# Performance work log

Measured on AMD Instinct MI355X. Metric: run time of the kernel, lower is better.

## Reference

```python
import jax, jax.numpy as jnp
import numpy as np

B, C, D, K = 65536, 128, 32, 10
EPS = 1e-12


def setup_inputs() -> dict:
    key = jax.random.key(0)
    k1, k2, k3, k4 = jax.random.split(key, 4)
    data = jax.random.normal(k1, (B, D), dtype=jnp.float32)
    mu = jax.random.normal(k2, (C, D), dtype=jnp.float32)
    # S_inv must be symmetric positive definite (inverse covariance per cluster)
    A = 0.1 * jax.random.normal(k3, (C, D, D), dtype=jnp.float32)
    S_inv = jnp.einsum('cij,ckj->cik', A, A) + jnp.eye(D, dtype=jnp.float32)[None]
    # one-hot class assignment per cluster (int32), as stored in the module
    cls = jax.random.randint(k4, (C,), 0, K)
    cluster_labels = jax.nn.one_hot(cls, K, dtype=jnp.int32)
    return {"data": data, "mu": mu, "S_inv": S_inv, "cluster_labels": cluster_labels}


def reference(data, mu, S_inv, cluster_labels):
    # Mahalanobis distance d2[b,c] = (z_b - mu_c)^T S_inv_c (z_b - mu_c),
    # expanded to avoid a [B, C, D] diff tensor.
    zz = data[:, :, None] * data[:, None, :]            # [B, D, D]
    t1 = jnp.einsum('bde,cde->bc', zz, S_inv)           # z' Sinv z
    Sm = jnp.einsum('cde,ce->cd', S_inv, mu)            # [C, D]
    t2 = data @ Sm.T                                    # z' Sinv mu  [B, C]
    t3 = jnp.einsum('cd,cd->c', mu, Sm)                 # mu' Sinv mu [C]
    d2 = t1 - 2.0 * t2 + t3[None, :]                    # [B, C]
    Gamma = jnp.exp(-0.5 * d2)                          # Gaussian activation
    # defuzzify_batch: normalize activations, project through one-hot labels
    norm_gamma = Gamma / (jnp.sum(Gamma, axis=1, keepdims=True) + EPS)
    label_scores = norm_gamma @ cluster_labels.astype(jnp.float32)  # [B, K]
    preds = jnp.argmax(label_scores, axis=1)
    clusters = jnp.argmax(Gamma, axis=1)
    return label_scores, preds, clusters
```

## Files before the change

### kernel.cpp

```cpp
#include <hip/hip_runtime.h>
#include <cmath>

#define B_N 65536
#define C_N 128
#define D_N 32
#define K_N 10
#define EPS_F 1e-12f
#define SCALE_F (-0.72134752044448169f)

#define NKK 48
#define CHUNK_F16 4096
#define QF_N (NKK * CHUNK_F16)
#define YSTR 33

typedef _Float16 f16x8 __attribute__((ext_vector_type(8)));
typedef float    f32x16 __attribute__((ext_vector_type(16)));

__device__ __forceinline__ void mdkk(int kk, int& dA, int& e0) {
    if (kk >= 45) { dA = 0; e0 = 0; return; }
    int w = (kk >= 17) + (kk >= 30) + (kk >= 39) + (kk >= 44);
    int off = w == 0 ? 0 : (w == 1 ? 17 : (w == 2 ? 30 : (w == 3 ? 39 : 44)));
    int r = kk - off;
    dA = 2 * r;
    e0 = 2 * r + 8 * w;
}

__global__ __launch_bounds__(128) void k_prep(const float* __restrict__ S,
                                              const float* __restrict__ mu,
                                              const int* __restrict__ onehot,
                                              _Float16* __restrict__ QF,
                                              int* __restrict__ cls) {
    const int c = blockIdx.x;
    const int tid = threadIdx.x;
    __shared__ float sSm[D_N];
    __shared__ float st3;

    if (tid < D_N) {
        const float* Sr = S + (size_t)c * (D_N * D_N) + (size_t)tid * D_N;
        const float* mr = mu + (size_t)c * D_N;
        float a0 = 0.f, a1 = 0.f;
#pragma unroll
        for (int e = 0; e < D_N; e += 2) {
            a0 = fmaf(Sr[e + 0], mr[e + 0], a0);
            a1 = fmaf(Sr[e + 1], mr[e + 1], a1);
        }
        sSm[tid] = a0 + a1;
    }
    __syncthreads();
    if (tid == 0) {
        const float* mr = mu + (size_t)c * D_N;
        float a = 0.f;
#pragma unroll
        for (int d = 0; d < D_N; ++d) a = fmaf(mr[d], sSm[d], a);
        st3 = a;
        int cl = 0;
#pragma unroll
        for (int k = 0; k < K_N; ++k)
            if (onehot[c * K_N + k] != 0) cl = k;
        cls[c] = cl;
    }
    __syncthreads();

    if (tid < 2 * NKK) {
        const int kk   = tid >> 1;
        const int half = tid & 1;
        int dA, e0;
        mdkk(kk, dA, e0);
        const int d  = dA + half;
        const int ct = c >> 5;
        const size_t base = (size_t)kk * CHUNK_F16 + ct * 1024
                          + (size_t)(half * 32 + (c & 31)) * 8;
        const float* Sc = S + (size_t)c * (D_N * D_N);
        for (int j = 0; j < 8; ++j) {
            const int e = e0 + j;
            float q = 0.f;
            if (kk < 45 && d <= e && e <= 32) {
                float v;
                if (e < 32)      v = Sc[d * D_N + e] * (d == e ? 1.f : 2.f);
                else if (d < 32) v = -2.f * sSm[d];
                else             v = st3;
                q = SCALE_F * v;
            }
            _Float16 h = (_Float16)q;
            QF[base + j]       = h;
            QF[base + 512 + j] = (_Float16)(q - (float)h);
        }
    }
}

__device__ __forceinline__ void gl_lds16(const void* g, void* l) {
    __builtin_amdgcn_global_load_lds(
        (const __attribute__((address_space(1))) unsigned int*)g,
        (__attribute__((address_space(3))) unsigned int*)l, 16, 0, 0);
}

__device__ __forceinline__ void stage_chunk(const _Float16* __restrict__ QF,
                                            _Float16* __restrict__ dst,
                                            int chunk, int wid, int lane) {
#pragma unroll
    for (int i = 0; i < 2; ++i) {
        const int slot = i * 4 + wid;
        gl_lds16(QF + (size_t)chunk * CHUNK_F16 + slot * 512 + lane * 8,
                 dst + slot * 512);
    }
}

__device__ __forceinline__ void ldy(const float* sy, int ybase, int hioff,
                                    int kk, float& yd, float (&yw)[8]) {
    int dA, e0;
    mdkk(kk, dA, e0);
    yd = sy[ybase + dA + hioff];
#pragma unroll
    for (int j = 0; j < 8; ++j) yw[j] = sy[ybase + e0 + j];
}

__device__ __forceinline__ void mkphi(float yd, const float (&yw)[8],
                                      f16x8& ph, f16x8& pl) {
    union { unsigned int w[4]; f16x8 v; } H, L;
#pragma unroll
    for (int p = 0; p < 4; ++p) {
        float f0 = yd * yw[2 * p], f1 = yd * yw[2 * p + 1];
        auto h2 = __builtin_amdgcn_cvt_pkrtz(f0, f1);
        float r0 = f0 - (float)h2[0];
        float r1 = f1 - (float)h2[1];
        auto l2 = __builtin_amdgcn_cvt_pkrtz(r0, r1);
        __builtin_memcpy(&H.w[p], &h2, 4);
        __builtin_memcpy(&L.w[p], &l2, 4);
    }
    ph = H.v;
    pl = L.v;
}

template <int SN, int SS, int P>
__device__ __forceinline__ void phase_t(int t, const _Float16* __restrict__ QF,
                                        _Float16* __restrict__ qb,
                                        const float* __restrict__ sy,
                                        int ybase, int hioff, int wid, int lane,
                                        f16x8 (&qh)[2][4], f16x8 (&ql)[2][4],
                                        float (&yd)[2], float (&yw)[2][8],
                                        f32x16 (&acc)[4]) {
    asm volatile("s_waitcnt vmcnt(0)" ::: "memory");
    __builtin_amdgcn_s_barrier();
    __builtin_amdgcn_sched_barrier(0);
    if (t + 2 < NKK)
        stage_chunk(QF, qb + SS * CHUNK_F16, t + 2, wid, lane);
    if (t + 1 < NKK) {
        const f16x8* qn = (const f16x8*)(qb + SN * CHUNK_F16);
#pragma unroll
        for (int ct = 0; ct < 4; ++ct) {
            qh[P ^ 1][ct] = qn[ct * 128 + lane];
            ql[P ^ 1][ct] = qn[ct * 128 + 64 + lane];
        }
        ldy(sy, ybase, hioff, t + 1, yd[P ^ 1], yw[P ^ 1]);
    }
    f16x8 ph, pl;
    mkphi(yd[P], yw[P], ph, pl);
    __builtin_amdgcn_s_setprio(1);
#pragma unroll
    for (int ct = 0; ct < 4; ++ct)
        acc[ct] = __builtin_amdgcn_mfma_f32_32x32x16_f16(qh[P][ct], ph, acc[ct], 0, 0, 0);
#pragma unroll
    for (int ct = 0; ct < 4; ++ct)
        acc[ct] = __builtin_amdgcn_mfma_f32_32x32x16_f16(ql[P][ct], ph, acc[ct], 0, 0, 0);
#pragma unroll
    for (int ct = 0; ct < 4; ++ct)
        acc[ct] = __builtin_amdgcn_mfma_f32_32x32x16_f16(qh[P][ct], pl, acc[ct], 0, 0, 0);
    __builtin_amdgcn_s_setprio(0);
}

__global__ __launch_bounds__(256, 2) void k_mainv9(const float* __restrict__ data,
                                                   const _Float16* __restrict__ QF,
                                                   const int* __restrict__ clsp,
                                                   float* __restrict__ out) {
    const int tid  = threadIdx.x;
    const int lane = tid & 63;
    const int wid  = tid >> 6;
    const int b0w  = blockIdx.x * 128 + wid * 32;
    const int col  = lane & 31;
    const bool hi  = lane >= 32;

    __shared__ float sy[256 * YSTR + 64];
    __shared__ alignas(16) _Float16 qb[4 * CHUNK_F16];
    __shared__ int lcls[C_N];
    if (tid < C_N) lcls[tid] = clsp[tid];

    const int ybase = tid * YSTR;
    {
        const float4* p0 = (const float4*)(data + (size_t)(b0w + col) * D_N);
#pragma unroll
        for (int i = 0; i < 8; ++i) {
            float4 v = p0[i];
            sy[ybase + 4 * i + 0] = v.x;
            sy[ybase + 4 * i + 1] = v.y;
            sy[ybase + 4 * i + 2] = v.z;
            sy[ybase + 4 * i + 3] = v.w;
        }
        sy[ybase + 32] = 1.f;
        if (tid < 64) sy[256 * YSTR + tid] = 0.f;
    }

    f32x16 acc[4];
#pragma unroll
    for (int ct = 0; ct < 4; ++ct)
#pragma unroll
        for (int g = 0; g < 16; ++g) acc[ct][g] = 0.f;

    stage_chunk(QF, qb + 0 * CHUNK_F16, 0, wid, lane);
    stage_chunk(QF, qb + 1 * CHUNK_F16, 1, wid, lane);
    __syncthreads();

    const int hioff = hi ? 1 : 0;
    f16x8 qh[2][4], ql[2][4];
    float yd[2], yw[2][8];
    {
        const f16x8* q0 = (const f16x8*)qb;
#pragma unroll
        for (int ct = 0; ct < 4; ++ct) {
            qh[0][ct] = q0[ct * 128 + lane];
            ql[0][ct] = q0[ct * 128 + 64 + lane];
        }
        ldy(sy, ybase, hioff, 0, yd[0], yw[0]);
    }

#pragma clang loop unroll(disable)
    for (int t = 0; t < NKK; t += 4) {
        phase_t<1, 2, 0>(t + 0, QF, qb, sy, ybase, hioff, wid, lane, qh, ql, yd, yw, acc);
        phase_t<2, 3, 1>(t + 1, QF, qb, sy, ybase, hioff, wid, lane, qh, ql, yd, yw, acc);
        phase_t<3, 0, 0>(t + 2, QF, qb, sy, ybase, hioff, wid, lane, qh, ql, yd, yw, acc);
        phase_t<0, 1, 1>(t + 3, QF, qb, sy, ybase, hioff, wid, lane, qh, ql, yd, yw, acc);
    }

    const float hoff = hi ? 4.f : 0.f;
    const int* lc = lcls + (hi ? 4 : 0);
    float sum = 0.f, gmax = -1.f, gcf = 0.f;
    float a0 = 0, a1 = 0, a2 = 0, a3 = 0, a4 = 0, a5 = 0, a6 = 0, a7 = 0, a8 = 0, a9 = 0;
#pragma unroll
    for (int ct = 0; ct < 4; ++ct) {
        float psum = 0.f;
#pragma unroll
        for (int g = 0; g < 16; ++g) {
            float v = acc[ct][g];
            float gm;
            asm("v_exp_f32 %0, %1" : "=v"(gm) : "v"(v));
            const int cbase = ct * 32 + (g & 3) + 8 * (g >> 2);
            int cl = lc[cbase];
            psum += gm;
            float cf = (float)cbase + hoff;
            if (gm > gmax) { gmax = gm; gcf = cf; }
            a0 += (cl == 0) ? gm : 0.f;
            a1 += (cl == 1) ? gm : 0.f;
            a2 += (cl == 2) ? gm : 0.f;
            a3 += (cl == 3) ? gm : 0.f;
            a4 += (cl == 4) ? gm : 0.f;
            a5 += (cl == 5) ? gm : 0.f;
            a6 += (cl == 6) ? gm : 0.f;
            a7 += (cl == 7) ? gm : 0.f;
            a8 += (cl == 8) ? gm : 0.f;
            a9 += (cl == 9) ? gm : 0.f;
        }
        sum += psum;
    }

    sum += __shfl_xor(sum, 32, 64);
    {
        float om = __shfl_xor(gmax, 32, 64);
        float oc = __shfl_xor(gcf, 32, 64);
        bool take = (om > gmax) || (om == gmax && oc < gcf);
        if (take) { gmax = om; gcf = oc; }
    }
    a0 += __shfl_xor(a0, 32, 64);
    a1 += __shfl_xor(a1, 32, 64);
    a2 += __shfl_xor(a2, 32, 64);
    a3 += __shfl_xor(a3, 32, 64);
    a4 += __shfl_xor(a4, 32, 64);
    a5 += __shfl_xor(a5, 32, 64);
    a6 += __shfl_xor(a6, 32, 64);
    a7 += __shfl_xor(a7, 32, 64);
    a8 += __shfl_xor(a8, 32, 64);
    a9 += __shfl_xor(a9, 32, 64);

    if (!hi) {
        const int b = b0w + col;
        float inv = 1.0f / (sum + EPS_F);
        float ls[K_N] = {a0 * inv, a1 * inv, a2 * inv, a3 * inv, a4 * inv,
                         a5 * inv, a6 * inv, a7 * inv, a8 * inv, a9 * inv};
        float best = -1.f;
        int bk = 0;
#pragma unroll
        for (int k = 0; k < K_N; ++k)
            if (ls[k] > best) { best = ls[k]; bk = k; }
        float2* o2 = (float2*)(out + (size_t)b * K_N);
#pragma unroll
        for (int k2 = 0; k2 < K_N / 2; ++k2)
            o2[k2] = make_float2(ls[2 * k2], ls[2 * k2 + 1]);
        out[(size_t)B_N * K_N + b] = (float)bk;
        out[(size_t)B_N * K_N + B_N + b] = gcf;
    }
}

extern "C" void kernel_launch(void* const* d_in, const int* in_sizes, int n_in,
                              void* d_out, int out_size, void* d_ws, size_t ws_size,
                              hipStream_t stream) {
    const float* data   = (const float*)d_in[0];
    const float* mu     = (const float*)d_in[1];
    const float* S      = (const float*)d_in[2];
    const int*   onehot = (const int*)d_in[3];
    float* out = (float*)d_out;

    _Float16* QF  = (_Float16*)d_ws;
    int*      cls = (int*)(QF + QF_N);

    hipLaunchKernelGGL(k_prep, dim3(C_N), dim3(128), 0, stream,
                       S, mu, onehot, QF, cls);
    hipLaunchKernelGGL(k_mainv9, dim3(B_N / 128), dim3(256), 0, stream,
                       data, QF, cls, out);
}
```

Before: 109.9 us.

## Split cluster columns across two waves per row group with 512-thread blocks

Blocks grow from 4 to 8 waves. Each pair of waves covers the same 32 rows but half of the 128 clusters, so each wave holds 2 accumulator tiles instead of 4 and more waves can be resident. The y operand loads become a sliding window that reuses the previous values instead of reloading 8 floats every step, and the software-pipelined register double buffering of Q fragments is removed. Partial sums, maxima and class sums from the two column halves are merged through a shared-memory scratch with an extra block barrier. Q staging now spreads one LDS load per wave across 8 waves.

```diff
diff --git a/kernel.cpp b/kernel.cpp
--- a/kernel.cpp
+++ b/kernel.cpp
@@ -94,26 +94,6 @@
         (__attribute__((address_space(3))) unsigned int*)l, 16, 0, 0);
 }
 
-__device__ __forceinline__ void stage_chunk(const _Float16* __restrict__ QF,
-                                            _Float16* __restrict__ dst,
-                                            int chunk, int wid, int lane) {
-#pragma unroll
-    for (int i = 0; i < 2; ++i) {
-        const int slot = i * 4 + wid;
-        gl_lds16(QF + (size_t)chunk * CHUNK_F16 + slot * 512 + lane * 8,
-                 dst + slot * 512);
-    }
-}
-
-__device__ __forceinline__ void ldy(const float* sy, int ybase, int hioff,
-                                    int kk, float& yd, float (&yw)[8]) {
-    int dA, e0;
-    mdkk(kk, dA, e0);
-    yd = sy[ybase + dA + hioff];
-#pragma unroll
-    for (int j = 0; j < 8; ++j) yw[j] = sy[ybase + e0 + j];
-}
-
 __device__ __forceinline__ void mkphi(float yd, const float (&yw)[8],
                                       f16x8& ph, f16x8& pl) {
     union { unsigned int w[4]; f16x8 v; } H, L;
@@ -131,103 +111,94 @@
     pl = L.v;
 }
 
-template <int SN, int SS, int P>
-__device__ __forceinline__ void phase_t(int t, const _Float16* __restrict__ QF,
-                                        _Float16* __restrict__ qb,
-                                        const float* __restrict__ sy,
-                                        int ybase, int hioff, int wid, int lane,
-                                        f16x8 (&qh)[2][4], f16x8 (&ql)[2][4],
-                                        float (&yd)[2], float (&yw)[2][8],
-                                        f32x16 (&acc)[4]) {
-    asm volatile("s_waitcnt vmcnt(0)" ::: "memory");
-    __builtin_amdgcn_s_barrier();
-    __builtin_amdgcn_sched_barrier(0);
-    if (t + 2 < NKK)
-        stage_chunk(QF, qb + SS * CHUNK_F16, t + 2, wid, lane);
-    if (t + 1 < NKK) {
-        const f16x8* qn = (const f16x8*)(qb + SN * CHUNK_F16);
-#pragma unroll
-        for (int ct = 0; ct < 4; ++ct) {
-            qh[P ^ 1][ct] = qn[ct * 128 + lane];
-            ql[P ^ 1][ct] = qn[ct * 128 + 64 + lane];
-        }
-        ldy(sy, ybase, hioff, t + 1, yd[P ^ 1], yw[P ^ 1]);
-    }
-    f16x8 ph, pl;
-    mkphi(yd[P], yw[P], ph, pl);
-    __builtin_amdgcn_s_setprio(1);
-#pragma unroll
-    for (int ct = 0; ct < 4; ++ct)
-        acc[ct] = __builtin_amdgcn_mfma_f32_32x32x16_f16(qh[P][ct], ph, acc[ct], 0, 0, 0);
-#pragma unroll
-    for (int ct = 0; ct < 4; ++ct)
-        acc[ct] = __builtin_amdgcn_mfma_f32_32x32x16_f16(ql[P][ct], ph, acc[ct], 0, 0, 0);
-#pragma unroll
-    for (int ct = 0; ct < 4; ++ct)
-        acc[ct] = __builtin_amdgcn_mfma_f32_32x32x16_f16(qh[P][ct], pl, acc[ct], 0, 0, 0);
-    __builtin_amdgcn_s_setprio(0);
-}
-
-__global__ __launch_bounds__(256, 2) void k_mainv9(const float* __restrict__ data,
-                                                   const _Float16* __restrict__ QF,
-                                                   const int* __restrict__ clsp,
-                                                   float* __restrict__ out) {
+__global__ __launch_bounds__(512, 4) void k_mainv10(const float* __restrict__ data,
+                                                    const _Float16* __restrict__ QF,
+                                                    const int* __restrict__ clsp,
+                                                    float* __restrict__ out) {
     const int tid  = threadIdx.x;
     const int lane = tid & 63;
     const int wid  = tid >> 6;
-    const int b0w  = blockIdx.x * 128 + wid * 32;
+    const int rg   = wid >> 1;
+    const int cg   = wid & 1;
     const int col  = lane & 31;
     const bool hi  = lane >= 32;
-
-    __shared__ float sy[256 * YSTR + 64];
+    const int bb   = blockIdx.x * 128;
+
+    __shared__ float sy[128 * YSTR + 64];
     __shared__ alignas(16) _Float16 qb[4 * CHUNK_F16];
     __shared__ int lcls[C_N];
+    __shared__ float scr[4][2][32][14];
+
     if (tid < C_N) lcls[tid] = clsp[tid];
-
-    const int ybase = tid * YSTR;
-    {
-        const float4* p0 = (const float4*)(data + (size_t)(b0w + col) * D_N);
+    if (tid < 128) {
+        const float4* p0 = (const float4*)(data + (size_t)(bb + tid) * D_N);
+        const int yb = tid * YSTR;
 #pragma unroll
         for (int i = 0; i < 8; ++i) {
             float4 v = p0[i];
-            sy[ybase + 4 * i + 0] = v.x;
-            sy[ybase + 4 * i + 1] = v.y;
-            sy[ybase + 4 * i + 2] = v.z;
-            sy[ybase + 4 * i + 3] = v.w;
-        }
-        sy[ybase + 32] = 1.f;
-        if (tid < 64) sy[256 * YSTR + tid] = 0.f;
-    }
-
-    f32x16 acc[4];
-#pragma unroll
-    for (int ct = 0; ct < 4; ++ct)
-#pragma unroll
-        for (int g = 0; g < 16; ++g) acc[ct][g] = 0.f;
-
-    stage_chunk(QF, qb + 0 * CHUNK_F16, 0, wid, lane);
-    stage_chunk(QF, qb + 1 * CHUNK_F16, 1, wid, lane);
+            sy[yb + 4 * i + 0] = v.x;
+            sy[yb + 4 * i + 1] = v.y;
+            sy[yb + 4 * i + 2] = v.z;
+            sy[yb + 4 * i + 3] = v.w;
+        }
+        sy[yb + 32] = 1.f;
+    } else if (tid < 192) {
+        sy[128 * YSTR + (tid - 128)] = 0.f;
+    }
+
+    f32x16 acc[2];
+#pragma unroll
+    for (int lt = 0; lt < 2; ++lt)
+#pragma unroll
+        for (int g = 0; g < 16; ++g) acc[lt][g] = 0.f;
+
+    gl_lds16(QF + 0 * CHUNK_F16 + wid * 512 + lane * 8, qb + 0 * CHUNK_F16 + wid * 512);
+    gl_lds16(QF + 1 * CHUNK_F16 + wid * 512 + lane * 8, qb + 1 * CHUNK_F16 + wid * 512);
     __syncthreads();
 
     const int hioff = hi ? 1 : 0;
-    f16x8 qh[2][4], ql[2][4];
-    float yd[2], yw[2][8];
-    {
-        const f16x8* q0 = (const f16x8*)qb;
-#pragma unroll
-        for (int ct = 0; ct < 4; ++ct) {
-            qh[0][ct] = q0[ct * 128 + lane];
-            ql[0][ct] = q0[ct * 128 + 64 + lane];
-        }
-        ldy(sy, ybase, hioff, 0, yd[0], yw[0]);
-    }
+    const float* yrow = sy + (rg * 32 + col) * YSTR;
+    float yw[8], yd = 0.f;
+    int e0 = 0, dAh = hioff;
 
 #pragma clang loop unroll(disable)
-    for (int t = 0; t < NKK; t += 4) {
-        phase_t<1, 2, 0>(t + 0, QF, qb, sy, ybase, hioff, wid, lane, qh, ql, yd, yw, acc);
-        phase_t<2, 3, 1>(t + 1, QF, qb, sy, ybase, hioff, wid, lane, qh, ql, yd, yw, acc);
-        phase_t<3, 0, 0>(t + 2, QF, qb, sy, ybase, hioff, wid, lane, qh, ql, yd, yw, acc);
-        phase_t<0, 1, 1>(t + 3, QF, qb, sy, ybase, hioff, wid, lane, qh, ql, yd, yw, acc);
+    for (int t = 0; t < NKK; ++t) {
+        asm volatile("s_waitcnt vmcnt(0)" ::: "memory");
+        __builtin_amdgcn_s_barrier();
+        __builtin_amdgcn_sched_barrier(0);
+        if (t + 2 < NKK)
+            gl_lds16(QF + (size_t)(t + 2) * CHUNK_F16 + wid * 512 + lane * 8,
+                     qb + ((t + 2) & 3) * CHUNK_F16 + wid * 512);
+
+        if (t == 0 || t == 17 || t == 30 || t == 39 || t == 44) {
+            e0  = (t == 0) ? 0 : (t == 17) ? 8 : (t == 30) ? 16 : (t == 39) ? 24 : 32;
+            dAh = hioff;
+#pragma unroll
+            for (int j = 0; j < 8; ++j) yw[j] = yrow[e0 + j];
+            yd = yrow[dAh];
+        } else if (t < 45) {
+            e0 += 2; dAh += 2;
+            yw[0] = yw[2]; yw[1] = yw[3]; yw[2] = yw[4];
+            yw[3] = yw[5]; yw[4] = yw[6]; yw[5] = yw[7];
+            yw[6] = yrow[e0 + 6];
+            yw[7] = yrow[e0 + 7];
+            yd = yrow[dAh];
+        }
+
+        const f16x8* qc = (const f16x8*)(qb + ((t & 3) * CHUNK_F16) + cg * 2048);
+        f16x8 qh0 = qc[lane],       ql0 = qc[64 + lane];
+        f16x8 qh1 = qc[128 + lane], ql1 = qc[192 + lane];
+
+        f16x8 ph, pl;
+        mkphi(yd, yw, ph, pl);
+        __builtin_amdgcn_s_setprio(1);
+        acc[0] = __builtin_amdgcn_mfma_f32_32x32x16_f16(qh0, ph, acc[0], 0, 0, 0);
+        acc[1] = __builtin_amdgcn_mfma_f32_32x32x16_f16(qh1, ph, acc[1], 0, 0, 0);
+        acc[0] = __builtin_amdgcn_mfma_f32_32x32x16_f16(ql0, ph, acc[0], 0, 0, 0);
+        acc[1] = __builtin_amdgcn_mfma_f32_32x32x16_f16(ql1, ph, acc[1], 0, 0, 0);
+        acc[0] = __builtin_amdgcn_mfma_f32_32x32x16_f16(qh0, pl, acc[0], 0, 0, 0);
+        acc[1] = __builtin_amdgcn_mfma_f32_32x32x16_f16(qh1, pl, acc[1], 0, 0, 0);
+        __builtin_amdgcn_s_setprio(0);
     }
 
     const float hoff = hi ? 4.f : 0.f;
@@ -235,14 +206,15 @@
     float sum = 0.f, gmax = -1.f, gcf = 0.f;
     float a0 = 0, a1 = 0, a2 = 0, a3 = 0, a4 = 0, a5 = 0, a6 = 0, a7 = 0, a8 = 0, a9 = 0;
 #pragma unroll
-    for (int ct = 0; ct < 4; ++ct) {
+    for (int lt = 0; lt < 2; ++lt) {
+        const int gt = cg * 2 + lt;
         float psum = 0.f;
 #pragma unroll
         for (int g = 0; g < 16; ++g) {
-            float v = acc[ct][g];
+            float v = acc[lt][g];
             float gm;
             asm("v_exp_f32 %0, %1" : "=v"(gm) : "v"(v));
-            const int cbase = ct * 32 + (g & 3) + 8 * (g >> 2);
+            const int cbase = gt * 32 + (g & 3) + 8 * (g >> 2);
             int cl = lc[cbase];
             psum += gm;
             float cf = (float)cbase + hoff;
@@ -280,21 +252,36 @@
     a9 += __shfl_xor(a9, 32, 64);
 
     if (!hi) {
-        const int b = b0w + col;
-        float inv = 1.0f / (sum + EPS_F);
-        float ls[K_N] = {a0 * inv, a1 * inv, a2 * inv, a3 * inv, a4 * inv,
-                         a5 * inv, a6 * inv, a7 * inv, a8 * inv, a9 * inv};
+        float* s = scr[rg][cg][col];
+        s[0] = sum; s[1] = gmax; s[2] = gcf;
+        s[3] = a0; s[4] = a1; s[5] = a2; s[6] = a3; s[7] = a4;
+        s[8] = a5; s[9] = a6; s[10] = a7; s[11] = a8; s[12] = a9;
+    }
+    __syncthreads();
+
+    if (cg == 0 && !hi) {
+        const float* s0 = scr[rg][0][col];
+        const float* s1 = scr[rg][1][col];
+        float fs = s0[0] + s1[0];
+        float gm = s0[1];
+        float gc = s0[2];
+        if (s1[1] > gm) { gm = s1[1]; gc = s1[2]; }
+        float inv = 1.0f / (fs + EPS_F);
+        float ls[K_N];
         float best = -1.f;
         int bk = 0;
 #pragma unroll
-        for (int k = 0; k < K_N; ++k)
+        for (int k = 0; k < K_N; ++k) {
+            ls[k] = (s0[3 + k] + s1[3 + k]) * inv;
             if (ls[k] > best) { best = ls[k]; bk = k; }
+        }
+        const int b = bb + rg * 32 + col;
         float2* o2 = (float2*)(out + (size_t)b * K_N);
 #pragma unroll
         for (int k2 = 0; k2 < K_N / 2; ++k2)
             o2[k2] = make_float2(ls[2 * k2], ls[2 * k2 + 1]);
         out[(size_t)B_N * K_N + b] = (float)bk;
-        out[(size_t)B_N * K_N + B_N + b] = gcf;
+        out[(size_t)B_N * K_N + B_N + b] = gc;
     }
 }
 
@@ -312,6 +299,6 @@
 
     hipLaunchKernelGGL(k_prep, dim3(C_N), dim3(128), 0, stream,
                        S, mu, onehot, QF, cls);
-    hipLaunchKernelGGL(k_mainv9, dim3(B_N / 128), dim3(256), 0, stream,
+    hipLaunchKernelGGL(k_mainv10, dim3(B_N / 128), dim3(512), 0, stream,
                        data, QF, cls, out);
 }
```

New measurement: 110.3 us. No clear change (+0.4%).
